# Optimization experiments

Measured on AMD Instinct MI355X. Metric: run time of the kernel, lower is better.

The kernel has to match this reference:

```python
import jax, jax.numpy as jnp
import numpy as np
import math

B, S, D = 2, 2048, 512
N_BUCKETS = 64
N_HYP = int(math.log2(N_BUCKETS))  # 6


def setup_inputs() -> dict:
    key = jax.random.key(0)
    ks = jax.random.split(key, 6)
    x = jax.random.normal(ks[0], (B, S, D), dtype=jnp.float32)
    # torch.nn.Linear params: weight [out,in], bias [out]
    Wq = jax.random.normal(ks[1], (D, D), dtype=jnp.float32) / jnp.sqrt(D)
    bq = jax.random.normal(ks[2], (D,), dtype=jnp.float32) * 0.01
    Wv = jax.random.normal(ks[3], (D, D), dtype=jnp.float32) / jnp.sqrt(D)
    bv = jax.random.normal(ks[4], (D,), dtype=jnp.float32) * 0.01
    hyperplanes = jax.random.normal(ks[5], (D + 1, N_HYP), dtype=jnp.float32)
    return {"x": x, "Wq": Wq, "bq": bq, "Wv": Wv, "bv": bv, "hyperplanes": hyperplanes}


def _get_buckets(q, hyperplanes):
    # append constant-1 feature: [B,S,D+1]
    qa = jnp.concatenate([q, jnp.ones(q.shape[:2] + (1,), q.dtype)], axis=2)
    proj = jnp.einsum('bse,en->bsn', qa, hyperplanes)
    bits = (proj >= 0).astype(jnp.float32)
    powers = (2.0 ** jnp.arange(N_HYP)).astype(jnp.float32)
    return jnp.einsum('bsn,n->bs', bits, powers)  # [B,S] float bucket ids


def reference(x, Wq, bq, Wv, bv, hyperplanes):
    q = x @ Wq.T + bq
    v = x @ Wv.T + bv
    buckets = _get_buckets(q, hyperplanes)  # [B,S]
    scale = 1.0 / math.sqrt(D)

    def body(acc, i):
        # NOTE: faithful to source: tokens IN bucket i are zeroed (masked_fill
        # with mask = buckets == i), then full dense softmax attention.
        mask = (buckets == i)[..., None]  # [B,S,1]
        qb = jnp.where(mask, 0.0, q)
        vb = jnp.where(mask, 0.0, v)
        att = jax.nn.softmax(jnp.einsum('bsd,btd->bst', qb, qb) * scale, axis=-1)
        return acc + jnp.einsum('bst,btd->bsd', att, vb), None

    init = jnp.zeros_like(x)
    out, _ = jax.lax.scan(body, init, jnp.arange(N_BUCKETS, dtype=jnp.float32))
    return out
```

## Files before the change

### kernel.cpp

```cpp
#include <hip/hip_runtime.h>
#include <math.h>

#define B_ 2
#define S_ 2048
#define D_ 512
#define NB_ 64
#define NH_ 6
#define ROWS (B_*S_)
#define SCALE 0.044194173824159216f

typedef float f32x4 __attribute__((ext_vector_type(4)));
typedef __bf16 bf16v8 __attribute__((ext_vector_type(8)));
typedef short s16x8 __attribute__((ext_vector_type(8)));
typedef unsigned short u16x4 __attribute__((ext_vector_type(4)));

__device__ __forceinline__ float b2f(unsigned short u) {
    unsigned int v = (unsigned int)u << 16;
    float f; __builtin_memcpy(&f, &v, 4); return f;
}
__device__ __forceinline__ unsigned short f2b(float f) {
    unsigned int v; __builtin_memcpy(&v, &f, 4);
    v += 0x7fffu + ((v >> 16) & 1u);
    return (unsigned short)(v >> 16);
}

#define GLOAD16(g, l) __builtin_amdgcn_global_load_lds( \
    (const __attribute__((address_space(1))) unsigned int*)(g), \
    (__attribute__((address_space(3))) unsigned int*)(uintptr_t)(l), 16, 0, 0)

__global__ void prep_kernel(
    const float* __restrict__ x, unsigned short* __restrict__ xh,
    const float* __restrict__ Wq, const float* __restrict__ Wv,
    unsigned short* __restrict__ Wqvh,
    float* __restrict__ Mrow, int* __restrict__ cnt, float* __restrict__ sumVall,
    float* __restrict__ out)
{
    int t = blockIdx.x * 256 + threadIdx.x;
    int stride = gridDim.x * 256;
    for (int i = t; i < ROWS * D_ / 4; i += stride) {
        float4 f = ((const float4*)x)[i];
        u16x4 u = { f2b(f.x), f2b(f.y), f2b(f.z), f2b(f.w) };
        ((u16x4*)xh)[i] = u;
        float4 z = {0.f, 0.f, 0.f, 0.f};
        ((float4*)out)[i] = z;
    }
    for (int i = t; i < D_ * D_ / 4; i += stride) {
        float4 f = ((const float4*)Wq)[i];
        u16x4 u = { f2b(f.x), f2b(f.y), f2b(f.z), f2b(f.w) };
        ((u16x4*)Wqvh)[i] = u;
        float4 g = ((const float4*)Wv)[i];
        u16x4 w = { f2b(g.x), f2b(g.y), f2b(g.z), f2b(g.w) };
        ((u16x4*)(Wqvh + (size_t)D_ * D_))[i] = w;
    }
    for (int i = t; i < ROWS; i += stride) Mrow[i] = 0.f;
    for (int i = t; i < B_ * NB_; i += stride) cnt[i] = 0;
    for (int i = t; i < B_ * D_; i += stride) sumVall[i] = 0.f;
}

__global__ __launch_bounds__(256) void mfma_proj(
    const unsigned short* __restrict__ A, const unsigned short* __restrict__ B,
    const float* __restrict__ bq, const float* __restrict__ bv,
    float* __restrict__ MrowRaw, unsigned short* __restrict__ qh,
    float* __restrict__ v)
{
    __shared__ unsigned short Als[128 * 64];
    __shared__ unsigned short Bls[64 * 64];
    const int K = D_;
    int tid = threadIdx.x;
    int w = tid >> 6, l = tid & 63;
    int wr = w >> 1, wc = w & 1;

    int gx = gridDim.x;
    int nwg = gx * gridDim.y;
    int lin = blockIdx.y * gx + blockIdx.x;
    int qq = nwg >> 3;
    int wg = (lin & 7) * qq + (lin >> 3);
    int m0 = (wg / gx) * 128, n0 = (wg % gx) * 64;

    const unsigned short* asrc[4];
    #pragma unroll
    for (int j = 0; j < 4; ++j) {
        int chunk = w * 4 + j;
        int r = chunk * 8 + (l >> 3);
        asrc[j] = A + (size_t)(m0 + r) * K + ((l & 7) ^ (l >> 3)) * 8;
    }
    const unsigned short* bsrc[2];
    #pragma unroll
    for (int j = 0; j < 2; ++j) {
        int chunk = w * 2 + j;
        int r = n0 + chunk * 8 + (l >> 3);
        bsrc[j] = B + (size_t)r * K + ((l & 7) ^ (l >> 3)) * 8;
    }

    f32x4 acc[4][2] = {};
    int rl = l & 15, hi = l >> 4;

    for (int k0 = 0; k0 < K; k0 += 64) {
        #pragma unroll
        for (int j = 0; j < 4; ++j) GLOAD16(asrc[j] + k0, Als + (w * 4 + j) * 512);
        #pragma unroll
        for (int j = 0; j < 2; ++j) GLOAD16(bsrc[j] + k0, Bls + (w * 2 + j) * 512);
        __syncthreads();
        bf16v8 af[4][2], bfr[2][2];
        const char* Ab = (const char*)Als;
        const char* Bb = (const char*)Bls;
        #pragma unroll
        for (int kk = 0; kk < 2; ++kk) {
            int kb = kk * 64 + hi * 16;
            #pragma unroll
            for (int f = 0; f < 4; ++f) {
                int ra = wr * 64 + f * 16 + rl;
                af[f][kk] = *(const bf16v8*)(Ab + ra * 128 + (kb ^ ((ra & 7) << 4)));
            }
            #pragma unroll
            for (int f = 0; f < 2; ++f) {
                int rb = wc * 32 + f * 16 + rl;
                bfr[f][kk] = *(const bf16v8*)(Bb + rb * 128 + (kb ^ ((rb & 7) << 4)));
            }
        }
        #pragma unroll
        for (int fm = 0; fm < 4; ++fm)
            #pragma unroll
            for (int fn = 0; fn < 2; ++fn)
                #pragma unroll
                for (int kk = 0; kk < 2; ++kk)
                    acc[fm][fn] = __builtin_amdgcn_mfma_f32_16x16x32_bf16(
                        af[fm][kk], bfr[fn][kk], acc[fm][fn], 0, 0, 0);
        __syncthreads();
    }

    int colBase = n0 + wc * 32;
    if (colBase < D_) {
        #pragma unroll
        for (int fm = 0; fm < 4; ++fm) {
            float p[4] = {0.f, 0.f, 0.f, 0.f};
            #pragma unroll
            for (int fn = 0; fn < 2; ++fn) {
                int col = colBase + fn * 16 + rl;
                float bs = bq[col];
                #pragma unroll
                for (int r = 0; r < 4; ++r) {
                    int row = m0 + wr * 64 + fm * 16 + hi * 4 + r;
                    float cv = acc[fm][fn][r] + bs;
                    unsigned short h = f2b(cv);
                    qh[(size_t)row * D_ + col] = h;
                    float qb = b2f(h);
                    p[r] = fmaf(qb, qb, p[r]);
                }
            }
            #pragma unroll
            for (int mask = 1; mask < 16; mask <<= 1)
                #pragma unroll
                for (int r = 0; r < 4; ++r) p[r] += __shfl_xor(p[r], mask);
            if (rl == 0) {
                #pragma unroll
                for (int r = 0; r < 4; ++r) {
                    int row = m0 + wr * 64 + fm * 16 + hi * 4 + r;
                    atomicAdd(&MrowRaw[row], p[r]);
                }
            }
        }
    } else {
        #pragma unroll
        for (int fm = 0; fm < 4; ++fm)
            #pragma unroll
            for (int fn = 0; fn < 2; ++fn) {
                int col = colBase + fn * 16 + rl - D_;
                float bs = bv[col];
                #pragma unroll
                for (int r = 0; r < 4; ++r) {
                    int row = m0 + wr * 64 + fm * 16 + hi * 4 + r;
                    v[(size_t)row * D_ + col] = acc[fm][fn][r] + bs;
                }
            }
    }
}

__global__ __launch_bounds__(256) void mfma_qk(
    const unsigned short* __restrict__ qh, const int* __restrict__ prm,
    const float* __restrict__ Mrow, unsigned short* __restrict__ Eh)
{
    __shared__ unsigned short Als[128 * 64];
    __shared__ unsigned short Bls[128 * 64];
    const int K = D_;
    int tid = threadIdx.x;
    int w = tid >> 6, l = tid & 63;
    int wr = w >> 1, wc = w & 1;
    int zb = blockIdx.z;
    const unsigned short* A = qh + (size_t)zb * S_ * D_;
    prm += (size_t)zb * S_;
    const float* Mb = Mrow + (size_t)zb * S_;
    unsigned short* Eb = Eh + (size_t)zb * S_ * S_;

    int gx = gridDim.x;
    int nwg = gx * gridDim.y;
    int lin = blockIdx.y * gx + blockIdx.x;
    int qq = nwg >> 3;
    int wg = (lin & 7) * qq + (lin >> 3);
    int m0 = (wg / gx) * 128, n0 = (wg % gx) * 128;

    const unsigned short* asrc[4];
    const unsigned short* bsrc[4];
    #pragma unroll
    for (int j = 0; j < 4; ++j) {
        int chunk = w * 4 + j;
        int r = chunk * 8 + (l >> 3);
        int c = ((l & 7) ^ (l >> 3)) * 8;
        asrc[j] = A + (size_t)(m0 + r) * K + c;
        bsrc[j] = A + (size_t)prm[n0 + r] * K + c;
    }

    f32x4 acc[4][4] = {};
    int rl = l & 15, hi = l >> 4;

    for (int k0 = 0; k0 < K; k0 += 64) {
        #pragma unroll
        for (int j = 0; j < 4; ++j) GLOAD16(asrc[j] + k0, Als + (w * 4 + j) * 512);
        #pragma unroll
        for (int j = 0; j < 4; ++j) GLOAD16(bsrc[j] + k0, Bls + (w * 4 + j) * 512);
        __syncthreads();
        bf16v8 af[4][2], bfr[4][2];
        const char* Ab = (const char*)Als;
        const char* Bb = (const char*)Bls;
        #pragma unroll
        for (int kk = 0; kk < 2; ++kk) {
            int kb = kk * 64 + hi * 16;
            #pragma unroll
            for (int f = 0; f < 4; ++f) {
                int ra = wr * 64 + f * 16 + rl;
                af[f][kk] = *(const bf16v8*)(Ab + ra * 128 + (kb ^ ((ra & 7) << 4)));
                int rb = wc * 64 + f * 16 + rl;
                bfr[f][kk] = *(const bf16v8*)(Bb + rb * 128 + (kb ^ ((rb & 7) << 4)));
            }
        }
        #pragma unroll
        for (int fm = 0; fm < 4; ++fm)
            #pragma unroll
            for (int fn = 0; fn < 4; ++fn)
                #pragma unroll
                for (int kk = 0; kk < 2; ++kk)
                    acc[fm][fn] = __builtin_amdgcn_mfma_f32_16x16x32_bf16(
                        af[fm][kk], bfr[fn][kk], acc[fm][fn], 0, 0, 0);
        __syncthreads();
    }

    #pragma unroll
    for (int fm = 0; fm < 4; ++fm) {
        #pragma unroll
        for (int r = 0; r < 4; ++r) {
            int row = m0 + wr * 64 + fm * 16 + hi * 4 + r;
            float m = Mb[row];
            #pragma unroll
            for (int fn = 0; fn < 4; ++fn) {
                int col = n0 + wc * 64 + fn * 16 + rl;
                float ev = __expf(fmaf(acc[fm][fn][r], SCALE, -m));
                Eb[(size_t)row * S_ + col] = f2b(ev);
            }
        }
    }
}

__global__ __launch_bounds__(256) void mfma_pv64(
    const unsigned short* __restrict__ Eh, const unsigned short* __restrict__ vT,
    const float* __restrict__ sumVall, const float* __restrict__ sumVb,
    const int* __restrict__ bucket, float* __restrict__ out)
{
    __shared__ unsigned short Als[64 * 64];
    __shared__ unsigned short Bls[64 * 64];
    int tid = threadIdx.x, w = tid >> 6, l = tid & 63;
    int wr = w >> 1, wc = w & 1, rl = l & 15, hi = l >> 4;
    int zb = blockIdx.z >> 1, kz = blockIdx.z & 1;
    const unsigned short* A  = Eh + (size_t)zb * S_ * S_;
    const unsigned short* Bv = vT + (size_t)zb * D_ * S_;
    const float* sva = sumVall + (size_t)zb * D_;
    const float* svb = sumVb + (size_t)zb * NB_ * D_;
    const int* bkt = bucket + (size_t)zb * S_;
    float* outb = out + (size_t)zb * S_ * D_;

    int lin = blockIdx.y * 8 + blockIdx.x;
    int xcd = lin & 7, rest = lin >> 3;
    int m0 = (((rest >> 3) << 3) | xcd) * 64;
    int n0 = (rest & 7) * 64;

    const unsigned short* asrc[2];
    const unsigned short* bsrc[2];
    #pragma unroll
    for (int j = 0; j < 2; ++j) {
        int chunk = w * 2 + j;
        int r = chunk * 8 + (l >> 3);
        int c = ((l & 7) ^ (l >> 3)) * 8;
        asrc[j] = A  + (size_t)(m0 + r) * S_ + c;
        bsrc[j] = Bv + (size_t)(n0 + r) * S_ + c;
    }

    f32x4 acc[2][2] = {};
    int kbeg = kz * (S_ / 2), kend = kbeg + S_ / 2;
    for (int k0 = kbeg; k0 < kend; k0 += 64) {
        #pragma unroll
        for (int j = 0; j < 2; ++j) GLOAD16(asrc[j] + k0, Als + (w * 2 + j) * 512);
        #pragma unroll
        for (int j = 0; j < 2; ++j) GLOAD16(bsrc[j] + k0, Bls + (w * 2 + j) * 512);
        __syncthreads();
        bf16v8 af[2][2], bfr[2][2];
        const char* Ab = (const char*)Als;
        const char* Bb = (const char*)Bls;
        #pragma unroll
        for (int kk = 0; kk < 2; ++kk) {
            int kb = kk * 64 + hi * 16;
            #pragma unroll
            for (int f = 0; f < 2; ++f) {
                int ra = wr * 32 + f * 16 + rl;
                af[f][kk] = *(const bf16v8*)(Ab + ra * 128 + (kb ^ ((ra & 7) << 4)));
                int rb = wc * 32 + f * 16 + rl;
                bfr[f][kk] = *(const bf16v8*)(Bb + rb * 128 + (kb ^ ((rb & 7) << 4)));
            }
        }
        #pragma unroll
        for (int fm = 0; fm < 2; ++fm)
            #pragma unroll
            for (int fn = 0; fn < 2; ++fn)
                #pragma unroll
                for (int kk = 0; kk < 2; ++kk)
                    acc[fm][fn] = __builtin_amdgcn_mfma_f32_16x16x32_bf16(
                        af[fm][kk], bfr[fn][kk], acc[fm][fn], 0, 0, 0);
        __syncthreads();
    }
    const float invS = 1.0f / (float)S_;
    #pragma unroll
    for (int fm = 0; fm < 2; ++fm)
        #pragma unroll
        for (int fn = 0; fn < 2; ++fn) {
            int col = n0 + wc * 32 + fn * 16 + rl;
            float sa = sva[col];
            #pragma unroll
            for (int r = 0; r < 4; ++r) {
                int row = m0 + wr * 32 + fm * 16 + hi * 4 + r;
                float val = acc[fm][fn][r];
                if (kz == 0) {
                    int bm = bkt[row];
                    val += (sa - svb[(size_t)bm * D_ + col]) * invS;
                }
                atomicAdd(&outb[(size_t)row * D_ + col], val);
            }
        }
}

__global__ __launch_bounds__(256) void vprep_kernel(
    const float* __restrict__ v, const int* __restrict__ perm,
    unsigned short* __restrict__ vT,
    const int* __restrict__ cnt, const int* __restrict__ idxl,
    float* __restrict__ sumVb, float* __restrict__ sumVall)
{
    int bid = blockIdx.x;
    if (bid < 2048) {
        __shared__ float tl[32][33];
        int b = bid >> 10;
        int r = bid & 1023;
        int d0 = (r & 15) * 32, s0 = (r >> 4) * 32;
        int tx = threadIdx.x & 31, ty = threadIdx.x >> 5;
        const float* vb = v + (size_t)b * S_ * D_;
        const int* pm = perm + (size_t)b * S_;
        #pragma unroll
        for (int i = 0; i < 4; ++i)
            tl[ty + i * 8][tx] = vb[(size_t)pm[s0 + ty + i * 8] * D_ + d0 + tx];
        __syncthreads();
        unsigned short* vt = vT + (size_t)b * D_ * S_;
        #pragma unroll
        for (int i = 0; i < 4; ++i)
            vt[(size_t)(d0 + ty + i * 8) * S_ + s0 + tx] = f2b(tl[tx][ty + i * 8]);
    } else {
        int sid = bid - 2048;
        int j = sid & 63, b = (sid >> 6) & 1, dblk = sid >> 7;
        int d = dblk * 256 + threadIdx.x;
        int n = cnt[b * NB_ + j];
        const int* lst = idxl + ((size_t)(b * NB_ + j)) * S_;
        const float* vb = v + (size_t)b * S_ * D_;
        float acc = 0.f;
        for (int k = 0; k < n; ++k)
            acc += vb[(size_t)lst[k] * D_ + d];
        sumVb[((size_t)b * NB_ + j) * D_ + d] = acc;
        atomicAdd(&sumVall[b * D_ + d], acc);
    }
}

__global__ __launch_bounds__(64) void bucket_kernel(
    const unsigned short* __restrict__ qh, const float* __restrict__ H,
    int* __restrict__ bucket, float* __restrict__ Mrow,
    int* __restrict__ cnt, int* __restrict__ idxl)
{
    int row = blockIdx.x;
    int lane = threadIdx.x;
    const unsigned short* qr = qh + (size_t)row * D_;
    float proj[NH_] = {};
    s16x8 qv8 = *(const s16x8*)(qr + lane * 8);
    #pragma unroll
    for (int i = 0; i < 8; ++i) {
        float qv = b2f((unsigned short)qv8[i]);
        int d = lane * 8 + i;
        #pragma unroll
        for (int n = 0; n < NH_; ++n)
            proj[n] = fmaf(qv, H[d * NH_ + n], proj[n]);
    }
    #pragma unroll
    for (int off = 32; off; off >>= 1) {
        #pragma unroll
        for (int n = 0; n < NH_; ++n) proj[n] += __shfl_down(proj[n], off);
    }
    if (lane == 0) {
        int bk = 0;
        #pragma unroll
        for (int n = 0; n < NH_; ++n) {
            float p = proj[n] + H[D_ * NH_ + n];
            if (p >= 0.f) bk |= (1 << n);
        }
        bucket[row] = bk;
        Mrow[row] = Mrow[row] * SCALE;
        int b = row >> 11, s = row & (S_ - 1);
        int pos = atomicAdd(&cnt[b * NB_ + bk], 1);
        idxl[((size_t)(b * NB_ + bk)) * S_ + pos] = s;
    }
}

__global__ __launch_bounds__(64) void permprefix_kernel(
    const int* __restrict__ cnt, const int* __restrict__ idxl,
    int* __restrict__ off, int* __restrict__ perm, int* __restrict__ p2b)
{
    int b = blockIdx.x;
    int j = threadIdx.x;
    int c = cnt[b * NB_ + j];
    int x = c;
    #pragma unroll
    for (int o = 1; o < 64; o <<= 1) {
        int y = __shfl_up(x, o);
        if (j >= o) x += y;
    }
    int o = x - c;
    off[b * (NB_ + 1) + j] = o;
    if (j == 63) off[b * (NB_ + 1) + 64] = x;
    const int* lst = idxl + ((size_t)(b * NB_ + j)) * S_;
    for (int k = 0; k < c; ++k) {
        perm[(size_t)b * S_ + o + k] = lst[k];
        p2b[(size_t)b * S_ + o + k] = j;
    }
}

__global__ __launch_bounds__(256) void zwgamma_kernel(
    unsigned short* __restrict__ Eh, const int* __restrict__ p2b,
    const int* __restrict__ off, const int* __restrict__ cnt,
    const int* __restrict__ bucket, const float* __restrict__ Mrow)
{
    int row = blockIdx.x;
    int b = row >> 11;
    __shared__ float er[S_];
    __shared__ float zl[NB_];
    __shared__ float wl[NB_ + 1];
    int tid = threadIdx.x;
    unsigned short* Er = Eh + (size_t)row * S_;
    int t0 = tid * 8;
    s16x8 ev = *(const s16x8*)(Er + t0);
    #pragma unroll
    for (int i = 0; i < 8; ++i)
        er[t0 + i] = b2f((unsigned short)ev[i]);
    __syncthreads();
    {
        int j = tid >> 2, sub = tid & 3;
        int lo = off[b * (NB_ + 1) + j], hiX = off[b * (NB_ + 1) + j + 1];
        float z = 0.f;
        for (int k = lo + sub; k < hiX; k += 4) z += er[k];
        z += __shfl_xor(z, 1);
        z += __shfl_xor(z, 2);
        if (sub == 0) zl[j] = z;
    }
    __syncthreads();
    if (tid < NB_) {
        int j = tid;
        float zj = zl[j];
        float ztot = zj;
        #pragma unroll
        for (int o = 32; o; o >>= 1) ztot += __shfl_xor(ztot, o);
        int bs = bucket[row];
        float em = __expf(-Mrow[row]);
        float wj = 0.f;
        if (j != bs) wj = 1.0f / (ztot - zj + (float)cnt[b * NB_ + j] * em);
        float Wt = wj;
        #pragma unroll
        for (int o = 32; o; o >>= 1) Wt += __shfl_xor(Wt, o);
        wl[j] = wj;
        if (j == 0) wl[NB_] = Wt;
    }
    __syncthreads();
    float Wt = wl[NB_];
    const int* pb = p2b + (size_t)b * S_ + t0;
    int4 b0 = *(const int4*)pb;
    int4 b1 = *(const int4*)(pb + 4);
    s16x8 ov;
    ov[0] = (short)f2b(er[t0 + 0] * (Wt - wl[b0.x]));
    ov[1] = (short)f2b(er[t0 + 1] * (Wt - wl[b0.y]));
    ov[2] = (short)f2b(er[t0 + 2] * (Wt - wl[b0.z]));
    ov[3] = (short)f2b(er[t0 + 3] * (Wt - wl[b0.w]));
    ov[4] = (short)f2b(er[t0 + 4] * (Wt - wl[b1.x]));
    ov[5] = (short)f2b(er[t0 + 5] * (Wt - wl[b1.y]));
    ov[6] = (short)f2b(er[t0 + 6] * (Wt - wl[b1.z]));
    ov[7] = (short)f2b(er[t0 + 7] * (Wt - wl[b1.w]));
    *(s16x8*)(Er + t0) = ov;
}

extern "C" void kernel_launch(void* const* d_in, const int* in_sizes, int n_in,
                              void* d_out, int out_size, void* d_ws, size_t ws_size,
                              hipStream_t stream) {
    (void)in_sizes; (void)n_in; (void)out_size; (void)ws_size;
    const float* x  = (const float*)d_in[0];
    const float* Wq = (const float*)d_in[1];
    const float* bq = (const float*)d_in[2];
    const float* Wv = (const float*)d_in[3];
    const float* bv = (const float*)d_in[4];
    const float* H  = (const float*)d_in[5];
    float* out = (float*)d_out;

    char* p = (char*)d_ws;
    auto alloc = [&](size_t bytes) -> char* {
        char* r = p; p += (bytes + 255) & ~(size_t)255; return r;
    };
    float* v       = (float*)alloc((size_t)ROWS * D_ * 4);
    float* Mrow    = (float*)alloc((size_t)ROWS * 4);
    float* sumVb   = (float*)alloc((size_t)B_ * NB_ * D_ * 4);
    float* sumVall = (float*)alloc((size_t)B_ * D_ * 4);
    int*   bucket  = (int*)alloc((size_t)ROWS * 4);
    int*   cnt     = (int*)alloc((size_t)B_ * NB_ * 4);
    int*   offb    = (int*)alloc((size_t)B_ * (NB_ + 1) * 4);
    int*   perm    = (int*)alloc((size_t)B_ * S_ * 4);
    int*   p2b     = (int*)alloc((size_t)B_ * S_ * 4);
    int*   idxl    = (int*)alloc((size_t)B_ * NB_ * S_ * 4);
    unsigned short* xh   = (unsigned short*)alloc((size_t)ROWS * D_ * 2);
    unsigned short* qh   = (unsigned short*)alloc((size_t)ROWS * D_ * 2);
    unsigned short* Wqvh = (unsigned short*)alloc((size_t)2 * D_ * D_ * 2);
    unsigned short* vTh  = (unsigned short*)alloc((size_t)B_ * D_ * S_ * 2);
    unsigned short* Eh   = (unsigned short*)alloc((size_t)B_ * S_ * S_ * 2);

    prep_kernel<<<2048, 256, 0, stream>>>(x, xh, Wq, Wv, Wqvh, Mrow, cnt, sumVall, out);
    mfma_proj<<<dim3(2 * D_ / 64, ROWS / 128, 1), 256, 0, stream>>>(
        xh, Wqvh, bq, bv, Mrow, qh, v);
    bucket_kernel<<<ROWS, 64, 0, stream>>>(qh, H, bucket, Mrow, cnt, idxl);
    permprefix_kernel<<<B_, 64, 0, stream>>>(cnt, idxl, offb, perm, p2b);
    vprep_kernel<<<2048 + 256, 256, 0, stream>>>(v, perm, vTh, cnt, idxl, sumVb, sumVall);
    mfma_qk<<<dim3(S_ / 128, S_ / 128, B_), 256, 0, stream>>>(qh, perm, Mrow, Eh);
    zwgamma_kernel<<<ROWS, 256, 0, stream>>>(Eh, p2b, offb, cnt, bucket, Mrow);
    mfma_pv64<<<dim3(D_ / 64, S_ / 64, B_ * 2), 256, 0, stream>>>(
        Eh, vTh, sumVall, sumVb, bucket, out);
}
```

Measured before the change: 117.8 us.

## Drop split-K atomics in PV GEMM, widen K tile, parallelize perm scatter

The PV GEMM no longer splits K across two blocks with atomicAdd. Each block now covers the full K range with 128-wide K tiles and writes its output directly. Because the output no longer accumulates, prep_kernel stops zeroing it. The permutation scatter now has all 64 threads copy each bucket's list cooperatively, instead of one thread per bucket looping serially. The cost is half the PV grid, which lowers occupancy and parallelism, and twice the LDS per block.

```diff
diff --git a/kernel.cpp b/kernel.cpp
--- a/kernel.cpp
+++ b/kernel.cpp
@@ -32,8 +32,7 @@
     const float* __restrict__ x, unsigned short* __restrict__ xh,
     const float* __restrict__ Wq, const float* __restrict__ Wv,
     unsigned short* __restrict__ Wqvh,
-    float* __restrict__ Mrow, int* __restrict__ cnt, float* __restrict__ sumVall,
-    float* __restrict__ out)
+    float* __restrict__ Mrow, int* __restrict__ cnt, float* __restrict__ sumVall)
 {
     int t = blockIdx.x * 256 + threadIdx.x;
     int stride = gridDim.x * 256;
@@ -41,8 +40,6 @@
         float4 f = ((const float4*)x)[i];
         u16x4 u = { f2b(f.x), f2b(f.y), f2b(f.z), f2b(f.w) };
         ((u16x4*)xh)[i] = u;
-        float4 z = {0.f, 0.f, 0.f, 0.f};
-        ((float4*)out)[i] = z;
     }
     for (int i = t; i < D_ * D_ / 4; i += stride) {
         float4 f = ((const float4*)Wq)[i];
@@ -265,11 +262,11 @@
     const float* __restrict__ sumVall, const float* __restrict__ sumVb,
     const int* __restrict__ bucket, float* __restrict__ out)
 {
-    __shared__ unsigned short Als[64 * 64];
-    __shared__ unsigned short Bls[64 * 64];
+    __shared__ unsigned short Als[64 * 128];
+    __shared__ unsigned short Bls[64 * 128];
     int tid = threadIdx.x, w = tid >> 6, l = tid & 63;
     int wr = w >> 1, wc = w & 1, rl = l & 15, hi = l >> 4;
-    int zb = blockIdx.z >> 1, kz = blockIdx.z & 1;
+    int zb = blockIdx.z;
     const unsigned short* A  = Eh + (size_t)zb * S_ * S_;
     const unsigned short* Bv = vT + (size_t)zb * D_ * S_;
     const float* sva = sumVall + (size_t)zb * D_;
@@ -282,47 +279,44 @@
     int m0 = (((rest >> 3) << 3) | xcd) * 64;
     int n0 = (rest & 7) * 64;
 
-    const unsigned short* asrc[2];
-    const unsigned short* bsrc[2];
-    #pragma unroll
-    for (int j = 0; j < 2; ++j) {
-        int chunk = w * 2 + j;
-        int r = chunk * 8 + (l >> 3);
-        int c = ((l & 7) ^ (l >> 3)) * 8;
-        asrc[j] = A  + (size_t)(m0 + r) * S_ + c;
-        bsrc[j] = Bv + (size_t)(n0 + r) * S_ + c;
+    const unsigned short* asrc[4];
+    const unsigned short* bsrc[4];
+    #pragma unroll
+    for (int j = 0; j < 4; ++j) {
+        int ch = w * 4 + j;
+        int r = ch * 4 + (l >> 4);
+        int c16 = (l & 15) ^ (r & 7);
+        asrc[j] = A  + (size_t)(m0 + r) * S_ + c16 * 8;
+        bsrc[j] = Bv + (size_t)(n0 + r) * S_ + c16 * 8;
     }
 
     f32x4 acc[2][2] = {};
-    int kbeg = kz * (S_ / 2), kend = kbeg + S_ / 2;
-    for (int k0 = kbeg; k0 < kend; k0 += 64) {
-        #pragma unroll
-        for (int j = 0; j < 2; ++j) GLOAD16(asrc[j] + k0, Als + (w * 2 + j) * 512);
-        #pragma unroll
-        for (int j = 0; j < 2; ++j) GLOAD16(bsrc[j] + k0, Bls + (w * 2 + j) * 512);
-        __syncthreads();
-        bf16v8 af[2][2], bfr[2][2];
+    for (int k0 = 0; k0 < S_; k0 += 128) {
+        #pragma unroll
+        for (int j = 0; j < 4; ++j) GLOAD16(asrc[j] + k0, Als + (w * 4 + j) * 512);
+        #pragma unroll
+        for (int j = 0; j < 4; ++j) GLOAD16(bsrc[j] + k0, Bls + (w * 4 + j) * 512);
+        __syncthreads();
         const char* Ab = (const char*)Als;
         const char* Bb = (const char*)Bls;
         #pragma unroll
-        for (int kk = 0; kk < 2; ++kk) {
-            int kb = kk * 64 + hi * 16;
+        for (int ks = 0; ks < 4; ++ks) {
+            int kb = ks * 64 + hi * 16;
+            bf16v8 af[2], bfr[2];
             #pragma unroll
             for (int f = 0; f < 2; ++f) {
                 int ra = wr * 32 + f * 16 + rl;
-                af[f][kk] = *(const bf16v8*)(Ab + ra * 128 + (kb ^ ((ra & 7) << 4)));
+                af[f] = *(const bf16v8*)(Ab + ra * 256 + (kb ^ ((ra & 7) << 4)));
                 int rb = wc * 32 + f * 16 + rl;
-                bfr[f][kk] = *(const bf16v8*)(Bb + rb * 128 + (kb ^ ((rb & 7) << 4)));
-            }
-        }
-        #pragma unroll
-        for (int fm = 0; fm < 2; ++fm)
-            #pragma unroll
-            for (int fn = 0; fn < 2; ++fn)
-                #pragma unroll
-                for (int kk = 0; kk < 2; ++kk)
+                bfr[f] = *(const bf16v8*)(Bb + rb * 256 + (kb ^ ((rb & 7) << 4)));
+            }
+            #pragma unroll
+            for (int fm = 0; fm < 2; ++fm)
+                #pragma unroll
+                for (int fn = 0; fn < 2; ++fn)
                     acc[fm][fn] = __builtin_amdgcn_mfma_f32_16x16x32_bf16(
-                        af[fm][kk], bfr[fn][kk], acc[fm][fn], 0, 0, 0);
+                        af[fm], bfr[fn], acc[fm][fn], 0, 0, 0);
+        }
         __syncthreads();
     }
     const float invS = 1.0f / (float)S_;
@@ -335,12 +329,9 @@
             #pragma unroll
             for (int r = 0; r < 4; ++r) {
                 int row = m0 + wr * 32 + fm * 16 + hi * 4 + r;
-                float val = acc[fm][fn][r];
-                if (kz == 0) {
-                    int bm = bkt[row];
-                    val += (sa - svb[(size_t)bm * D_ + col]) * invS;
-                }
-                atomicAdd(&outb[(size_t)row * D_ + col], val);
+                int bm = bkt[row];
+                outb[(size_t)row * D_ + col] =
+                    acc[fm][fn][r] + (sa - svb[(size_t)bm * D_ + col]) * invS;
             }
         }
 }
@@ -427,6 +418,7 @@
 {
     int b = blockIdx.x;
     int j = threadIdx.x;
+    __shared__ int offs[NB_ + 1];
     int c = cnt[b * NB_ + j];
     int x = c;
     #pragma unroll
@@ -434,13 +426,19 @@
         int y = __shfl_up(x, o);
         if (j >= o) x += y;
     }
-    int o = x - c;
-    off[b * (NB_ + 1) + j] = o;
+    offs[j] = x - c;
+    if (j == 63) offs[64] = x;
+    off[b * (NB_ + 1) + j] = x - c;
     if (j == 63) off[b * (NB_ + 1) + 64] = x;
-    const int* lst = idxl + ((size_t)(b * NB_ + j)) * S_;
-    for (int k = 0; k < c; ++k) {
-        perm[(size_t)b * S_ + o + k] = lst[k];
-        p2b[(size_t)b * S_ + o + k] = j;
+    __syncthreads();
+    for (int jj = 0; jj < NB_; ++jj) {
+        int o = offs[jj];
+        int c2 = offs[jj + 1] - o;
+        const int* lst = idxl + ((size_t)(b * NB_ + jj)) * S_;
+        for (int k = j; k < c2; k += 64) {
+            perm[(size_t)b * S_ + o + k] = lst[k];
+            p2b[(size_t)b * S_ + o + k] = jj;
+        }
     }
 }
 
@@ -537,7 +535,7 @@
     unsigned short* vTh  = (unsigned short*)alloc((size_t)B_ * D_ * S_ * 2);
     unsigned short* Eh   = (unsigned short*)alloc((size_t)B_ * S_ * S_ * 2);
 
-    prep_kernel<<<2048, 256, 0, stream>>>(x, xh, Wq, Wv, Wqvh, Mrow, cnt, sumVall, out);
+    prep_kernel<<<2048, 256, 0, stream>>>(x, xh, Wq, Wv, Wqvh, Mrow, cnt, sumVall);
     mfma_proj<<<dim3(2 * D_ / 64, ROWS / 128, 1), 256, 0, stream>>>(
         xh, Wqvh, bq, bv, Mrow, qh, v);
     bucket_kernel<<<ROWS, 64, 0, stream>>>(qh, H, bucket, Mrow, cnt, idxl);
@@ -545,6 +543,6 @@
     vprep_kernel<<<2048 + 256, 256, 0, stream>>>(v, perm, vTh, cnt, idxl, sumVb, sumVall);
     mfma_qk<<<dim3(S_ / 128, S_ / 128, B_), 256, 0, stream>>>(qh, perm, Mrow, Eh);
     zwgamma_kernel<<<ROWS, 256, 0, stream>>>(Eh, p2b, offb, cnt, bucket, Mrow);
-    mfma_pv64<<<dim3(D_ / 64, S_ / 64, B_ * 2), 256, 0, stream>>>(
+    mfma_pv64<<<dim3(D_ / 64, S_ / 64, B_), 256, 0, stream>>>(
         Eh, vTh, sumVall, sumVb, bucket, out);
 }
```

Result: slower. 126.8 us (+7.6%).

## Drop split-K in PV GEMM and parallelize permutation scatter across threads

Applied to the files above, without the earlier changes.

The PV GEMM kernel no longer splits the K dimension into two halves combined with atomicAdd. Each block now runs the full K loop and writes its output with plain stores, so zeroing `out` in the prep kernel is no longer needed. The permutation-build kernel now uses 256 threads per batch, with four threads per bucket copying index lists in a strided loop after a shared-memory prefix scan. The trade-off is half as many PV blocks (512 instead of 1024), each with a K loop twice as long, in exchange for removing atomics and the output memset.

```diff
diff --git a/kernel.cpp b/kernel.cpp
--- a/kernel.cpp
+++ b/kernel.cpp
@@ -32,8 +32,7 @@
     const float* __restrict__ x, unsigned short* __restrict__ xh,
     const float* __restrict__ Wq, const float* __restrict__ Wv,
     unsigned short* __restrict__ Wqvh,
-    float* __restrict__ Mrow, int* __restrict__ cnt, float* __restrict__ sumVall,
-    float* __restrict__ out)
+    float* __restrict__ Mrow, int* __restrict__ cnt, float* __restrict__ sumVall)
 {
     int t = blockIdx.x * 256 + threadIdx.x;
     int stride = gridDim.x * 256;
@@ -41,8 +40,6 @@
         float4 f = ((const float4*)x)[i];
         u16x4 u = { f2b(f.x), f2b(f.y), f2b(f.z), f2b(f.w) };
         ((u16x4*)xh)[i] = u;
-        float4 z = {0.f, 0.f, 0.f, 0.f};
-        ((float4*)out)[i] = z;
     }
     for (int i = t; i < D_ * D_ / 4; i += stride) {
         float4 f = ((const float4*)Wq)[i];
@@ -269,7 +266,7 @@
     __shared__ unsigned short Bls[64 * 64];
     int tid = threadIdx.x, w = tid >> 6, l = tid & 63;
     int wr = w >> 1, wc = w & 1, rl = l & 15, hi = l >> 4;
-    int zb = blockIdx.z >> 1, kz = blockIdx.z & 1;
+    int zb = blockIdx.z;
     const unsigned short* A  = Eh + (size_t)zb * S_ * S_;
     const unsigned short* Bv = vT + (size_t)zb * D_ * S_;
     const float* sva = sumVall + (size_t)zb * D_;
@@ -294,8 +291,7 @@
     }
 
     f32x4 acc[2][2] = {};
-    int kbeg = kz * (S_ / 2), kend = kbeg + S_ / 2;
-    for (int k0 = kbeg; k0 < kend; k0 += 64) {
+    for (int k0 = 0; k0 < S_; k0 += 64) {
         #pragma unroll
         for (int j = 0; j < 2; ++j) GLOAD16(asrc[j] + k0, Als + (w * 2 + j) * 512);
         #pragma unroll
@@ -335,12 +331,9 @@
             #pragma unroll
             for (int r = 0; r < 4; ++r) {
                 int row = m0 + wr * 32 + fm * 16 + hi * 4 + r;
-                float val = acc[fm][fn][r];
-                if (kz == 0) {
-                    int bm = bkt[row];
-                    val += (sa - svb[(size_t)bm * D_ + col]) * invS;
-                }
-                atomicAdd(&outb[(size_t)row * D_ + col], val);
+                int bm = bkt[row];
+                outb[(size_t)row * D_ + col] =
+                    acc[fm][fn][r] + (sa - svb[(size_t)bm * D_ + col]) * invS;
             }
         }
 }
@@ -421,24 +414,31 @@
     }
 }
 
-__global__ __launch_bounds__(64) void permprefix_kernel(
+__global__ __launch_bounds__(256) void permprefix_kernel(
     const int* __restrict__ cnt, const int* __restrict__ idxl,
     int* __restrict__ off, int* __restrict__ perm, int* __restrict__ p2b)
 {
     int b = blockIdx.x;
-    int j = threadIdx.x;
-    int c = cnt[b * NB_ + j];
-    int x = c;
-    #pragma unroll
-    for (int o = 1; o < 64; o <<= 1) {
-        int y = __shfl_up(x, o);
-        if (j >= o) x += y;
-    }
-    int o = x - c;
-    off[b * (NB_ + 1) + j] = o;
-    if (j == 63) off[b * (NB_ + 1) + 64] = x;
+    int tid = threadIdx.x;
+    __shared__ int offs[NB_ + 1];
+    if (tid < 64) {
+        int c = cnt[b * NB_ + tid];
+        int x = c;
+        #pragma unroll
+        for (int o = 1; o < 64; o <<= 1) {
+            int y = __shfl_up(x, o);
+            if (tid >= o) x += y;
+        }
+        offs[tid] = x - c;
+        off[b * (NB_ + 1) + tid] = x - c;
+        if (tid == 63) { offs[64] = x; off[b * (NB_ + 1) + 64] = x; }
+    }
+    __syncthreads();
+    int j = tid >> 2, sub = tid & 3;
+    int o = offs[j];
+    int c2 = offs[j + 1] - o;
     const int* lst = idxl + ((size_t)(b * NB_ + j)) * S_;
-    for (int k = 0; k < c; ++k) {
+    for (int k = sub; k < c2; k += 4) {
         perm[(size_t)b * S_ + o + k] = lst[k];
         p2b[(size_t)b * S_ + o + k] = j;
     }
@@ -537,14 +537,14 @@
     unsigned short* vTh  = (unsigned short*)alloc((size_t)B_ * D_ * S_ * 2);
     unsigned short* Eh   = (unsigned short*)alloc((size_t)B_ * S_ * S_ * 2);
 
-    prep_kernel<<<2048, 256, 0, stream>>>(x, xh, Wq, Wv, Wqvh, Mrow, cnt, sumVall, out);
+    prep_kernel<<<2048, 256, 0, stream>>>(x, xh, Wq, Wv, Wqvh, Mrow, cnt, sumVall);
     mfma_proj<<<dim3(2 * D_ / 64, ROWS / 128, 1), 256, 0, stream>>>(
         xh, Wqvh, bq, bv, Mrow, qh, v);
     bucket_kernel<<<ROWS, 64, 0, stream>>>(qh, H, bucket, Mrow, cnt, idxl);
-    permprefix_kernel<<<B_, 64, 0, stream>>>(cnt, idxl, offb, perm, p2b);
+    permprefix_kernel<<<B_, 256, 0, stream>>>(cnt, idxl, offb, perm, p2b);
     vprep_kernel<<<2048 + 256, 256, 0, stream>>>(v, perm, vTh, cnt, idxl, sumVb, sumVall);
     mfma_qk<<<dim3(S_ / 128, S_ / 128, B_), 256, 0, stream>>>(qh, perm, Mrow, Eh);
     zwgamma_kernel<<<ROWS, 256, 0, stream>>>(Eh, p2b, offb, cnt, bucket, Mrow);
-    mfma_pv64<<<dim3(D_ / 64, S_ / 64, B_ * 2), 256, 0, stream>>>(
+    mfma_pv64<<<dim3(D_ / 64, S_ / 64, B_), 256, 0, stream>>>(
         Eh, vTh, sumVall, sumVb, bucket, out);
 }
```

Result: faster. 106.5 us, median of 2 (-9.6%).
